# Kernel optimization log

Hardware: AMD Instinct MI355X
Metric: run time of the kernel (lower is better)

Reference implementation:

```python
import jax, jax.numpy as jnp
import numpy as np

NUM_HEADS = 8
NUM_LAYERS = 4
BASE_THR = 0.5     # AdaptiveLIF base_threshold (state reset -> no adaptation on single step)
TAU_MEM = 5.0      # tau_mem (single step from zero state: mem = decay*0 + x = x)
SURR_SLOPE = 5.0   # fast-sigmoid surrogate slope (forward path unaffected)
EPS = 1e-5
NEG = -1e9


@jax.custom_vjp
def spike(u):
    return (u > 0.0).astype(u.dtype)

def _spike_fwd(u):
    return (u > 0.0).astype(u.dtype), u

def _spike_bwd(u, g):
    return (g / (1.0 + SURR_SLOPE * jnp.abs(u)) ** 2,)

spike.defvjp(_spike_fwd, _spike_bwd)


def lif(x):
    # AdaptiveLIF, single timestep from reset state: mem = x, thr = base_threshold
    return spike(x - BASE_THR)


def layer_norm(x, g, b):
    m = jnp.mean(x, axis=-1, keepdims=True)
    v = jnp.mean((x - m) ** 2, axis=-1, keepdims=True)
    return (x - m) * jax.lax.rsqrt(v + EPS) * g + b


def dsa(x, wq, bq, wk, bk, wv, bv, wo, bo, top_k):
    # Dynamic Sparse Attention: dense scores -> per-query top-k mask -> softmax -> AV
    B, T, D = x.shape
    H = NUM_HEADS
    dh = D // H

    def heads(w, bias):
        return (x @ w.T + bias).reshape(B, T, H, dh).transpose(0, 2, 1, 3)  # [B,H,T,dh]

    q, k, v = heads(wq, bq), heads(wk, bk), heads(wv, bv)
    scores = jnp.einsum('bhqd,bhkd->bhqk', q, k) / jnp.sqrt(jnp.asarray(dh, x.dtype))
    vals, idx = jax.lax.top_k(scores, top_k)  # [B,H,T,K]

    # scatter top-k values into a -inf-filled score matrix (exact top-k sparsity)
    N = B * H * T
    rows = jnp.arange(N)[:, None]
    sp = jnp.full((N, T), NEG, scores.dtype).at[rows, idx.reshape(N, top_k)].set(vals.reshape(N, top_k))
    attn = jax.nn.softmax(sp.reshape(B, H, T, T), axis=-1)

    out = jnp.einsum('bhqk,bhkd->bhqd', attn, v)
    out = out.transpose(0, 2, 1, 3).reshape(B, T, D)
    out = out @ wo.T + bo
    return lif(out)  # spiking output of attention


def ffn(x, w1, b1, w2, b2):
    h = lif(x @ w1.T + b1)
    return lif(h @ w2.T + b2)


def setup_inputs() -> dict:
    key = jax.random.key(0)
    ks = jax.random.split(key, 16)
    L, D, F, IN, OUT, B, T = NUM_LAYERS, 512, 2048, 128, 256, 2, 2048
    s = 0.02
    return {
        'x': jax.random.normal(ks[0], (B, T, IN), jnp.float32),
        'emb_w': jax.random.normal(ks[1], (D, IN), jnp.float32) * s,
        'emb_b': jnp.zeros((D,), jnp.float32),
        'pos_emb': jax.random.normal(ks[2], (1, T, D), jnp.float32) * s,
        'wq': jax.random.normal(ks[3], (L, D, D), jnp.float32) * s,
        'bq': jnp.zeros((L, D), jnp.float32),
        'wk': jax.random.normal(ks[4], (L, D, D), jnp.float32) * s,
        'bk': jnp.zeros((L, D), jnp.float32),
        'wv': jax.random.normal(ks[5], (L, D, D), jnp.float32) * s,
        'bv': jnp.zeros((L, D), jnp.float32),
        'wo': jax.random.normal(ks[6], (L, D, D), jnp.float32) * s,
        'bo': jnp.zeros((L, D), jnp.float32),
        'ln1_g': jnp.ones((L, D), jnp.float32),
        'ln1_b': jnp.zeros((L, D), jnp.float32),
        'fc1_w': jax.random.normal(ks[7], (L, F, D), jnp.float32) * s,
        'fc1_b': jnp.zeros((L, F), jnp.float32),
        'fc2_w': jax.random.normal(ks[8], (L, D, F), jnp.float32) * s,
        'fc2_b': jnp.zeros((L, D), jnp.float32),
        'ln2_g': jnp.ones((L, D), jnp.float32),
        'ln2_b': jnp.zeros((L, D), jnp.float32),
        'fnorm_g': jnp.ones((D,), jnp.float32),
        'fnorm_b': jnp.zeros((D,), jnp.float32),
        'cls_w': jax.random.normal(ks[9], (OUT, D), jnp.float32) * s,
        'cls_b': jnp.zeros((OUT,), jnp.float32),
        'top_k': 32,
    }


def reference(x, emb_w, emb_b, pos_emb, wq, bq, wk, bk, wv, bv, wo, bo,
              ln1_g, ln1_b, fc1_w, fc1_b, fc2_w, fc2_b, ln2_g, ln2_b,
              fnorm_g, fnorm_b, cls_w, cls_b, top_k):
    B, T, _ = x.shape
    h = x @ emb_w.T + emb_b + pos_emb[:, :T, :]
    for l in range(NUM_LAYERS):
        a = dsa(h, wq[l], bq[l], wk[l], bk[l], wv[l], bv[l], wo[l], bo[l], top_k)
        h = layer_norm(h + a, ln1_g[l], ln1_b[l])
        f = ffn(h, fc1_w[l], fc1_b[l], fc2_w[l], fc2_b[l])
        h = layer_norm(h + f, ln2_g[l], ln2_b[l])
    h = layer_norm(h, fnorm_g, fnorm_b)
    pooled = jnp.mean(h, axis=1)  # [B, D]
    return pooled @ cls_w.T + cls_b
```

## Files before the change

### kernel.cpp

```cpp
#include <hip/hip_runtime.h>
#include <math.h>
#include <float.h>

#define T_SEQ  2048
#define DMODEL 512
#define NHEAD  8
#define DHEAD  64
#define FDIM   2048
#define NLAYER 4
#define NB     2
#define MROWS  (NB*T_SEQ)

typedef _Float16 f16x8 __attribute__((ext_vector_type(8)));
typedef float    f32x4 __attribute__((ext_vector_type(4)));

__device__ __forceinline__ void async16(const _Float16* g, _Float16* l) {
    __builtin_amdgcn_global_load_lds(
        (const __attribute__((address_space(1))) unsigned int*)g,
        (__attribute__((address_space(3))) unsigned int*)l, 16, 0, 0);
}

template<int BN, int EPI>
__global__ __launch_bounds__(256) void gemm_k(
    const float* __restrict__ A, const float* __restrict__ W,
    const float* __restrict__ bias, const float* __restrict__ pos,
    float* __restrict__ C, int M, int N, int K)
{
    constexpr int BM = 128;
    constexpr int BK = 32;
    constexpr int MN = BN / 16;
    __shared__ float As[BK][BM + 4];
    __shared__ float Ws[BK][BN + 4];
    const int tid = threadIdx.x;
    const int n0 = blockIdx.x * BN;
    const int m0 = blockIdx.y * BM;
    const int tx = tid & 15;
    const int ty = tid >> 4;

    float acc[8][MN];
    #pragma unroll
    for (int i = 0; i < 8; ++i)
        #pragma unroll
        for (int j = 0; j < MN; ++j) acc[i][j] = 0.f;

    for (int k0 = 0; k0 < K; k0 += BK) {
        #pragma unroll
        for (int it = 0; it < 4; ++it) {
            int qq = tid + 256 * it;
            int m = qq >> 3, kq = qq & 7;
            float4 v4 = *(const float4*)(A + (size_t)(m0 + m) * K + k0 + kq * 4);
            As[kq*4+0][m] = v4.x; As[kq*4+1][m] = v4.y;
            As[kq*4+2][m] = v4.z; As[kq*4+3][m] = v4.w;
        }
        #pragma unroll
        for (int it = 0; it < BN/32; ++it) {
            int qq = tid + 256 * it;
            int n = qq >> 3, kq = qq & 7;
            float4 v4 = *(const float4*)(W + (size_t)(n0 + n) * K + k0 + kq * 4);
            Ws[kq*4+0][n] = v4.x; Ws[kq*4+1][n] = v4.y;
            Ws[kq*4+2][n] = v4.z; Ws[kq*4+3][n] = v4.w;
        }
        __syncthreads();
        for (int kk = 0; kk < BK; ++kk) {
            float a[8], b[MN];
            float4 a0 = *(const float4*)&As[kk][ty*8];
            float4 a1 = *(const float4*)&As[kk][ty*8+4];
            a[0]=a0.x; a[1]=a0.y; a[2]=a0.z; a[3]=a0.w;
            a[4]=a1.x; a[5]=a1.y; a[6]=a1.z; a[7]=a1.w;
            float4 b0 = *(const float4*)&Ws[kk][tx*4];
            b[0]=b0.x; b[1]=b0.y; b[2]=b0.z; b[3]=b0.w;
            if constexpr (MN == 8) {
                float4 b1 = *(const float4*)&Ws[kk][64 + tx*4];
                b[4]=b1.x; b[5]=b1.y; b[6]=b1.z; b[7]=b1.w;
            }
            #pragma unroll
            for (int i = 0; i < 8; ++i)
                #pragma unroll
                for (int j = 0; j < MN; ++j)
                    acc[i][j] = fmaf(a[i], b[j], acc[i][j]);
        }
        __syncthreads();
    }

    #pragma unroll
    for (int i = 0; i < 8; ++i) {
        int m = m0 + ty*8 + i;
        #pragma unroll
        for (int jb = 0; jb < MN/4; ++jb) {
            int nn = n0 + jb*64 + tx*4;
            float4 r;
            r.x = acc[i][jb*4+0] + bias[nn+0];
            r.y = acc[i][jb*4+1] + bias[nn+1];
            r.z = acc[i][jb*4+2] + bias[nn+2];
            r.w = acc[i][jb*4+3] + bias[nn+3];
            if constexpr (EPI == 1) {
                const float* pp = pos + (size_t)(m & (T_SEQ-1)) * DMODEL + nn;
                r.x += pp[0]; r.y += pp[1]; r.z += pp[2]; r.w += pp[3];
            }
            *(float4*)(C + (size_t)m * N + nn) = r;
        }
    }
}

template<int BM, int BN, int ASRC, int EPI, int LAYOUT>
__global__ __launch_bounds__(256, (BM == 64) ? 3 : 2) void mgemm_k(
    const _Float16* __restrict__ AH, const _Float16* __restrict__ AL,
    const _Float16* __restrict__ WH, const _Float16* __restrict__ WL,
    const float* __restrict__ bias,
    float* __restrict__ O0, float* __restrict__ O1, float* __restrict__ O2,
    float* __restrict__ O3, float* __restrict__ O4,
    int M, int N, int K)
{
    constexpr int MI = BM / 32;
    constexpr int NJ = BN / 32;
    __shared__ _Float16 AsH[2][4][BM][8];
    __shared__ _Float16 AsL[(ASRC == 0) ? 2 : 1][(ASRC == 0) ? 4 : 1][(ASRC == 0) ? BM : 1][8];
    __shared__ _Float16 WsH[2][4][BN][8];
    __shared__ _Float16 WsL[2][4][BN][8];

    const int tid = threadIdx.x;
    const int npan = N / BN;
    const int bid  = blockIdx.x;
    const int n0 = (bid % npan) * BN;
    const int m0 = (bid / npan) * BM;
    const int wv = tid >> 6, lane = tid & 63;
    const int mw = (wv >> 1) * (BM/2), nw = (wv & 1) * (BN/2);
    const int fr = lane & 15;
    const int kb = lane >> 4;

    const int wsrow = tid >> 1;
    const int wskb  = (tid & 1) * 2;
    const int wkoff = (tid & 1) * 16;
    const int arow  = tid >> 2, akb = tid & 3;

    f16x8 pa0, pa1, pal0, pal1, pw0, pw1, pwl0, pwl1;

    auto gload = [&](int k0) {
        if constexpr (BM == 128) {
            const _Float16* ap = AH + (size_t)(m0 + wsrow) * K + k0 + wkoff;
            pa0 = *(const f16x8*)ap;
            pa1 = *(const f16x8*)(ap + 8);
            if constexpr (ASRC == 0) {
                const _Float16* alp = AL + (size_t)(m0 + wsrow) * K + k0 + wkoff;
                pal0 = *(const f16x8*)alp;
                pal1 = *(const f16x8*)(alp + 8);
            }
        } else {
            pa0 = *(const f16x8*)(AH + (size_t)(m0 + arow) * K + k0 + akb*8);
            if constexpr (ASRC == 0)
                pal0 = *(const f16x8*)(AL + (size_t)(m0 + arow) * K + k0 + akb*8);
        }
        if constexpr (BN == 128) {
            const _Float16* wp = WH + (size_t)(n0 + wsrow) * K + k0 + wkoff;
            pw0 = *(const f16x8*)wp;
            pw1 = *(const f16x8*)(wp + 8);
            const _Float16* wlp = WL + (size_t)(n0 + wsrow) * K + k0 + wkoff;
            pwl0 = *(const f16x8*)wlp;
            pwl1 = *(const f16x8*)(wlp + 8);
        } else {
            pw0  = *(const f16x8*)(WH + (size_t)(n0 + arow) * K + k0 + akb*8);
            pwl0 = *(const f16x8*)(WL + (size_t)(n0 + arow) * K + k0 + akb*8);
        }
    };
    auto swrite = [&](int buf) {
        if constexpr (BM == 128) {
            *(f16x8*)&AsH[buf][wskb  ][wsrow][0] = pa0;
            *(f16x8*)&AsH[buf][wskb+1][wsrow][0] = pa1;
            if constexpr (ASRC == 0) {
                *(f16x8*)&AsL[buf][wskb  ][wsrow][0] = pal0;
                *(f16x8*)&AsL[buf][wskb+1][wsrow][0] = pal1;
            }
        } else {
            *(f16x8*)&AsH[buf][akb][arow][0] = pa0;
            if constexpr (ASRC == 0)
                *(f16x8*)&AsL[buf][akb][arow][0] = pal0;
        }
        if constexpr (BN == 128) {
            *(f16x8*)&WsH[buf][wskb  ][wsrow][0] = pw0;
            *(f16x8*)&WsH[buf][wskb+1][wsrow][0] = pw1;
            *(f16x8*)&WsL[buf][wskb  ][wsrow][0] = pwl0;
            *(f16x8*)&WsL[buf][wskb+1][wsrow][0] = pwl1;
        } else {
            *(f16x8*)&WsH[buf][akb][arow][0] = pw0;
            *(f16x8*)&WsL[buf][akb][arow][0] = pwl0;
        }
    };

    f32x4 acc[MI][NJ];
    #pragma unroll
    for (int i = 0; i < MI; ++i)
        #pragma unroll
        for (int j = 0; j < NJ; ++j) acc[i][j] = (f32x4)(0.f);

    const int NT = K >> 5;
    int cur = 0;
    gload(0);
    swrite(0);
    __syncthreads();

    for (int t = 0; t < NT; ++t) {
        const bool more = (t + 1 < NT);
        if (more) gload((t + 1) << 5);

        f16x8 aH[MI], aL[MI], bH[NJ], bL[NJ];
        #pragma unroll
        for (int i = 0; i < MI; ++i) {
            aH[i] = *(const f16x8*)&AsH[cur][kb][mw + i*16 + fr][0];
            if constexpr (ASRC == 0) aL[i] = *(const f16x8*)&AsL[cur][kb][mw + i*16 + fr][0];
        }
        #pragma unroll
        for (int j = 0; j < NJ; ++j) {
            bH[j] = *(const f16x8*)&WsH[cur][kb][nw + j*16 + fr][0];
            bL[j] = *(const f16x8*)&WsL[cur][kb][nw + j*16 + fr][0];
        }
        #pragma unroll
        for (int i = 0; i < MI; ++i)
            #pragma unroll
            for (int j = 0; j < NJ; ++j) {
                acc[i][j] = __builtin_amdgcn_mfma_f32_16x16x32_f16(aH[i], bH[j], acc[i][j], 0, 0, 0);
                acc[i][j] = __builtin_amdgcn_mfma_f32_16x16x32_f16(aH[i], bL[j], acc[i][j], 0, 0, 0);
                if constexpr (ASRC == 0)
                    acc[i][j] = __builtin_amdgcn_mfma_f32_16x16x32_f16(aL[i], bH[j], acc[i][j], 0, 0, 0);
            }
        if (more) {
            swrite(cur ^ 1);
            __syncthreads();
            cur ^= 1;
        }
    }

    const int qq = lane >> 4;
    #pragma unroll
    for (int j = 0; j < NJ; ++j) {
        int n = n0 + nw + j*16 + fr;
        float bv = bias[n];
        #pragma unroll
        for (int i = 0; i < MI; ++i) {
            #pragma unroll
            for (int r = 0; r < 4; ++r) {
                int m = m0 + mw + i*16 + qq*4 + r;
                float val = acc[i][j][r] * (1.f/1024.f) + bv;
                if constexpr (EPI == 2) val = val > 0.5f ? 1.f : 0.f;
                if constexpr (EPI == 3) {
                    ((_Float16*)O0)[(size_t)m * N + n] = (val > 0.5f) ? (_Float16)16.f : (_Float16)0.f;
                } else if constexpr (LAYOUT == 0) {
                    O0[(size_t)m * N + n] = val;
                } else {
                    int b_ = m >> 11, t_ = m & (T_SEQ-1);
                    if (n < 512) {
                        size_t hl = (((size_t)(b_*NHEAD + (n>>6))*T_SEQ + t_) << 6) + (n & 63);
                        float s16 = 16.f * val;
                        _Float16 hh = (_Float16)s16;
                        ((_Float16*)O0)[hl] = hh;
                        ((_Float16*)O1)[hl] = (_Float16)(s16 - (float)hh);
                    } else if (n < 1024) {
                        int nn = n - 512;
                        size_t hl = (((size_t)(b_*NHEAD + (nn>>6))*T_SEQ + t_) << 6) + (nn & 63);
                        float s16 = 16.f * val;
                        _Float16 hh = (_Float16)s16;
                        ((_Float16*)O2)[hl] = hh;
                        ((_Float16*)O3)[hl] = (_Float16)(s16 - (float)hh);
                    } else {
                        int nn = n - 1024;
                        O4[(((size_t)(b_*NHEAD + (nn>>6))*T_SEQ + t_) << 6) + (nn & 63)] = val;
                    }
                }
            }
        }
    }
}

__global__ __launch_bounds__(256) void cvtw_k(
    const float* __restrict__ w, _Float16* __restrict__ H, _Float16* __restrict__ L,
    int n, float scale)
{
    int i = blockIdx.x * 256 + threadIdx.x;
    if (i < n) {
        float s = scale * w[i];
        _Float16 h = (_Float16)s;
        H[i] = h;
        L[i] = (_Float16)(s - (float)h);
    }
}

__global__ __launch_bounds__(256) void cvtlayer_k(
    const float* __restrict__ wq, const float* __restrict__ wk, const float* __restrict__ wv,
    const float* __restrict__ bq, const float* __restrict__ bk, const float* __restrict__ bv,
    const float* __restrict__ wo, const float* __restrict__ f1w, const float* __restrict__ f2w,
    _Float16* __restrict__ WcatH, _Float16* __restrict__ WcatL, float* __restrict__ bcat,
    _Float16* __restrict__ WoH, _Float16* __restrict__ WoL,
    _Float16* __restrict__ W1H, _Float16* __restrict__ W1L,
    _Float16* __restrict__ W2H, _Float16* __restrict__ W2L)
{
    int i = blockIdx.x * 256 + threadIdx.x;
    float w;
    _Float16 *H, *L;
    int off;
    if (i < 786432) {
        int src = i >> 18, o = i & 262143;
        w = (src == 0 ? wq : (src == 1 ? wk : wv))[o];
        H = WcatH; L = WcatL; off = i;
    } else if (i < 1048576) {
        off = i - 786432;  w = wo[off];  H = WoH; L = WoL;
    } else if (i < 2097152) {
        off = i - 1048576; w = f1w[off]; H = W1H; L = W1L;
    } else if (i < 3145728) {
        off = i - 2097152; w = f2w[off]; H = W2H; L = W2L;
    } else if (i < 3145728 + 1536) {
        int j = i - 3145728;
        int src = j >> 9, o = j & 511;
        bcat[j] = (src == 0 ? bq : (src == 1 ? bk : bv))[o];
        return;
    } else return;
    float s = 64.f * w;
    _Float16 h = (_Float16)s;
    H[off] = h;
    L[off] = (_Float16)(s - (float)h);
}

__global__ __launch_bounds__(512, 4) void attn_k(
    const _Float16* __restrict__ qH, const _Float16* __restrict__ qL,
    const _Float16* __restrict__ kH, const _Float16* __restrict__ kL,
    const float* __restrict__ v,
    _Float16* __restrict__ outH, _Float16* __restrict__ outL)
{
    __shared__ unsigned char lds[66560];
    _Float16* ksH = (_Float16*)(lds);
    _Float16* ksL = (_Float16*)(lds + 16384);
    float    (*ss)[132] = (float(*)[132])(lds + 32768);
    float*   wrow       = (float*)(lds + 32768);
    int*     irow       = (int*)(lds + 32768 + 8448);

    const int tid = threadIdx.x;
    const int bh  = blockIdx.y;
    const int t0  = blockIdx.x * 64;
    const _Float16* qHb = qH + ((size_t)bh * T_SEQ + t0) * DHEAD;
    const _Float16* qLb = qL + ((size_t)bh * T_SEQ + t0) * DHEAD;
    const _Float16* kHb = kH + (size_t)bh * T_SEQ * DHEAD;
    const _Float16* kLb = kL + (size_t)bh * T_SEQ * DHEAD;
    const float*    vb  = v  + (size_t)bh * T_SEQ * DHEAD;

    unsigned kreg[32];
    #pragma unroll
    for (int i = 0; i < 32; ++i) kreg[i] = 0u;

    const int wv = tid >> 6, lane = tid & 63;
    const int fr = lane & 15, q4 = lane >> 4;
    const int mh  = (wv >> 2) * 32;
    const int c0w = (wv & 3) * 32;
    const int srow = tid >> 3;
    const int ssub = tid & 7;

    f16x8 qaH[2][2], qaL[2][2];
    #pragma unroll
    for (int ks = 0; ks < 2; ++ks) {
        const int doff = ks*32 + q4*8;
        qaH[ks][0] = *(const f16x8*)(qHb + (mh + fr)*DHEAD + doff);
        qaH[ks][1] = *(const f16x8*)(qHb + (mh + 16 + fr)*DHEAD + doff);
        qaL[ks][0] = *(const f16x8*)(qLb + (mh + fr)*DHEAD + doff);
        qaL[ks][1] = *(const f16x8*)(qLb + (mh + 16 + fr)*DHEAD + doff);
    }

    auto stage = [&](int jt) {
        const int j0 = jt * 128;
        #pragma unroll
        for (int i = 0; i < 2; ++i) {
            const int r0 = wv*16 + i*8;
            const int cc = r0 + (lane >> 3);
            const int ch = (lane & 7) ^ (cc & 7);
            const size_t goff = (size_t)(j0 + cc) * DHEAD + ch*8;
            async16(kHb + goff, ksH + r0*64);
            async16(kLb + goff, ksL + r0*64);
        }
    };

    stage(0);
    __syncthreads();

    for (int jt = 0; jt < 16; ++jt) {
        const int j0 = jt * 128;

        f32x4 acc[2][2];
        acc[0][0] = (f32x4)(0.f); acc[0][1] = (f32x4)(0.f);
        acc[1][0] = (f32x4)(0.f); acc[1][1] = (f32x4)(0.f);
        #pragma unroll
        for (int ks = 0; ks < 2; ++ks) {
            const int chq  = ks*4 + q4;
            #pragma unroll
            for (int nj = 0; nj < 2; ++nj) {
                const int cc = c0w + nj*16 + fr;
                const int sl = cc*64 + (chq ^ (cc & 7))*8;
                f16x8 bHf = *(const f16x8*)&ksH[sl];
                f16x8 bLf = *(const f16x8*)&ksL[sl];
                acc[0][nj] = __builtin_amdgcn_mfma_f32_16x16x32_f16(qaH[ks][0], bHf, acc[0][nj], 0, 0, 0);
                acc[0][nj] = __builtin_amdgcn_mfma_f32_16x16x32_f16(qaH[ks][0], bLf, acc[0][nj], 0, 0, 0);
                acc[0][nj] = __builtin_amdgcn_mfma_f32_16x16x32_f16(qaL[ks][0], bHf, acc[0][nj], 0, 0, 0);
                acc[1][nj] = __builtin_amdgcn_mfma_f32_16x16x32_f16(qaH[ks][1], bHf, acc[1][nj], 0, 0, 0);
                acc[1][nj] = __builtin_amdgcn_mfma_f32_16x16x32_f16(qaH[ks][1], bLf, acc[1][nj], 0, 0, 0);
                acc[1][nj] = __builtin_amdgcn_mfma_f32_16x16x32_f16(qaL[ks][1], bHf, acc[1][nj], 0, 0, 0);
            }
        }
        #pragma unroll
        for (int mi = 0; mi < 2; ++mi)
            #pragma unroll
            for (int nj = 0; nj < 2; ++nj)
                #pragma unroll
                for (int r = 0; r < 4; ++r)
                    ss[mh + mi*16 + q4*4 + r][c0w + nj*16 + fr] = acc[mi][nj][r] * (1.f/2048.f);
        __syncthreads();

        if (jt < 15) stage(jt + 1);

        float4 c4[4];
        {
            const float* ssr = &ss[srow][0] + ssub*4;
            #pragma unroll
            for (int g = 0; g < 4; ++g) c4[g] = *(const float4*)(ssr + g*32);
        }
        unsigned cand[16];
        #pragma unroll
        for (int g = 0; g < 4; ++g) {
            float vg[4] = {c4[g].x, c4[g].y, c4[g].z, c4[g].w};
            #pragma unroll
            for (int r = 0; r < 4; ++r) {
                unsigned u = __float_as_uint(vg[r]);
                u ^= (unsigned)((int)u >> 31) | 0x80000000u;
                int col = ssub*4 + g*32 + r;
                cand[g*4+r] = (u & 0xFFFFF800u) | (unsigned)(2047 - (j0 + col));
            }
        }
        #pragma unroll
        for (int k2 = 2; k2 <= 16; k2 <<= 1) {
            #pragma unroll
            for (int j2 = k2 >> 1; j2 > 0; j2 >>= 1) {
                #pragma unroll
                for (int i2 = 0; i2 < 16; ++i2) {
                    int l2 = i2 ^ j2;
                    if (l2 > i2) {
                        unsigned a = cand[i2], b = cand[l2];
                        unsigned mn = a < b ? a : b;
                        unsigned mx = a < b ? b : a;
                        if ((i2 & k2) == 0) { cand[i2] = mx; cand[l2] = mn; }
                        else                { cand[i2] = mn; cand[l2] = mx; }
                    }
                }
            }
        }
        #pragma unroll
        for (int j2 = 0; j2 < 16; ++j2) {
            unsigned b = cand[15 - j2];
            if (kreg[16 + j2] < b) kreg[16 + j2] = b;
        }
        #pragma unroll
        for (int st = 16; st >= 1; st >>= 1) {
            #pragma unroll
            for (int i2 = 0; i2 < 32; ++i2) {
                if ((i2 & st) == 0) {
                    unsigned lo = kreg[i2], hi = kreg[i2 | st];
                    kreg[i2]      = lo < hi ? hi : lo;
                    kreg[i2 | st] = lo < hi ? lo : hi;
                }
            }
        }
        __syncthreads();
    }

    #pragma unroll
    for (int s = 1; s <= 4; s <<= 1) {
        #pragma unroll
        for (int i = 0; i < 16; ++i) {
            unsigned pa = (unsigned)__shfl_xor((int)kreg[31-i], s, 64);
            unsigned pb = (unsigned)__shfl_xor((int)kreg[i],    s, 64);
            if (pa > kreg[i])    kreg[i]    = pa;
            if (pb > kreg[31-i]) kreg[31-i] = pb;
        }
        #pragma unroll
        for (int st = 16; st >= 1; st >>= 1) {
            #pragma unroll
            for (int i2 = 0; i2 < 32; ++i2) {
                if ((i2 & st) == 0) {
                    unsigned lo = kreg[i2], hi = kreg[i2 | st];
                    kreg[i2]      = lo < hi ? hi : lo;
                    kreg[i2 | st] = lo < hi ? lo : hi;
                }
            }
        }
    }

    if (ssub == 0) {
        float w[32];
        #pragma unroll
        for (int i = 0; i < 32; ++i) {
            unsigned um = kreg[i] & 0xFFFFF800u;
            unsigned ub = (um & 0x80000000u) ? (um ^ 0x80000000u) : ~um;
            w[i] = __uint_as_float(ub);
        }
        float m = w[0];
        float s = 0.f;
        #pragma unroll
        for (int i = 0; i < 32; ++i) { w[i] = __expf(w[i] - m); s += w[i]; }
        float inv = 1.f / s;
        #pragma unroll
        for (int i = 0; i < 32; ++i) {
            wrow[srow*33 + i] = w[i] * inv;
            irow[srow*33 + i] = 2047 - (int)(kreg[i] & 0x7FFu);
        }
    }
    __syncthreads();

    const int wid = tid >> 6, lane2 = tid & 63;
    const int b = bh >> 3, h = bh & 7;
    for (int rr = wid; rr < 64; rr += 8) {
        float a0 = 0.f, a1 = 0.f, a2 = 0.f, a3 = 0.f;
        #pragma unroll
        for (int i = 0; i < 8; ++i) {
            a0 = fmaf(wrow[rr*33 + i],      vb[(size_t)irow[rr*33 + i]      * DHEAD + lane2], a0);
            a1 = fmaf(wrow[rr*33 + 8 + i],  vb[(size_t)irow[rr*33 + 8 + i]  * DHEAD + lane2], a1);
            a2 = fmaf(wrow[rr*33 + 16 + i], vb[(size_t)irow[rr*33 + 16 + i] * DHEAD + lane2], a2);
            a3 = fmaf(wrow[rr*33 + 24 + i], vb[(size_t)irow[rr*33 + 24 + i] * DHEAD + lane2], a3);
        }
        float accv = (a0 + a1) + (a2 + a3);
        size_t oi = ((size_t)(b * T_SEQ + t0 + rr)) * DMODEL + h * DHEAD + lane2;
        float s16 = 16.f * accv;
        _Float16 hh = (_Float16)s16;
        outH[oi] = hh;
        outL[oi] = (_Float16)(s16 - (float)hh);
    }
}

__global__ __launch_bounds__(256) void ln_k(
    const float* __restrict__ x, const float* __restrict__ res,
    const float* __restrict__ g, const float* __restrict__ bb,
    float* __restrict__ out, _Float16* __restrict__ oH, _Float16* __restrict__ oL)
{
    __shared__ float red[8];
    const int row = blockIdx.x;
    const int tid = threadIdx.x;
    const float* xr = x + (size_t)row * DMODEL;
    float v0 = xr[tid], v1 = xr[tid + 256];
    if (res) {
        const float* rr = res + (size_t)row * DMODEL;
        v0 += rr[tid]; v1 += rr[tid + 256];
    }
    float s = v0 + v1;
    #pragma unroll
    for (int o = 1; o < 64; o <<= 1) s += __shfl_xor(s, o);
    const int wid = tid >> 6, lane = tid & 63;
    if (lane == 0) red[wid] = s;
    __syncthreads();
    float mean = (red[0] + red[1] + red[2] + red[3]) * (1.f / DMODEL);
    float d0 = v0 - mean, d1 = v1 - mean;
    float qs = d0*d0 + d1*d1;
    #pragma unroll
    for (int o = 1; o < 64; o <<= 1) qs += __shfl_xor(qs, o);
    if (lane == 0) red[4 + wid] = qs;
    __syncthreads();
    float var = (red[4] + red[5] + red[6] + red[7]) * (1.f / DMODEL);
    float rs = rsqrtf(var + 1e-5f);
    float o0 = d0 * rs * g[tid]       + bb[tid];
    float o1 = d1 * rs * g[tid + 256] + bb[tid + 256];
    size_t base = (size_t)row * DMODEL;
    out[base + tid]       = o0;
    out[base + tid + 256] = o1;
    float s0 = 16.f * o0, s1 = 16.f * o1;
    _Float16 h0 = (_Float16)s0, h1 = (_Float16)s1;
    oH[base + tid]       = h0;
    oH[base + tid + 256] = h1;
    oL[base + tid]       = (_Float16)(s0 - (float)h0);
    oL[base + tid + 256] = (_Float16)(s1 - (float)h1);
}

__global__ __launch_bounds__(256) void pool_k(
    const float* __restrict__ h, float* __restrict__ part)
{
    const int chunk = blockIdx.x & 15;
    const int idx = (blockIdx.x >> 4) * 256 + threadIdx.x;
    const int b = idx >> 9, d = idx & 511;
    const float* p = h + ((size_t)b * T_SEQ + chunk * 128) * DMODEL + d;
    float s = 0.f;
    for (int t = 0; t < 128; ++t) s += p[(size_t)t * DMODEL];
    part[chunk * 1024 + idx] = s;
}

__global__ __launch_bounds__(256) void poolsum_k(
    const float* __restrict__ part, float* __restrict__ pooled)
{
    int idx = blockIdx.x * 256 + threadIdx.x;
    float s = 0.f;
    #pragma unroll
    for (int c = 0; c < 16; ++c) s += part[c * 1024 + idx];
    pooled[idx] = s * (1.f / T_SEQ);
}

__global__ __launch_bounds__(256) void cls_k(
    const float* __restrict__ pooled, const float* __restrict__ w,
    const float* __restrict__ bias, float* __restrict__ out)
{
    const int wid = threadIdx.x >> 6, lane = threadIdx.x & 63;
    const int oi = blockIdx.x * 4 + wid;
    const int b = oi >> 8, o = oi & 255;
    const float* pr = pooled + b * DMODEL;
    const float* wr = w + (size_t)o * DMODEL;
    float s = 0.f;
    for (int d = lane; d < DMODEL; d += 64) s = fmaf(pr[d], wr[d], s);
    #pragma unroll
    for (int off = 1; off < 64; off <<= 1) s += __shfl_xor(s, off);
    if (lane == 0) out[oi] = s + bias[o];
}

extern "C" void kernel_launch(void* const* d_in, const int* in_sizes, int n_in,
                              void* d_out, int out_size, void* d_ws, size_t ws_size,
                              hipStream_t stream)
{
    const float* x     = (const float*)d_in[0];
    const float* emb_w = (const float*)d_in[1];
    const float* emb_b = (const float*)d_in[2];
    const float* pos   = (const float*)d_in[3];
    const float* wq    = (const float*)d_in[4];
    const float* bq    = (const float*)d_in[5];
    const float* wk    = (const float*)d_in[6];
    const float* bk    = (const float*)d_in[7];
    const float* wv    = (const float*)d_in[8];
    const float* bv    = (const float*)d_in[9];
    const float* wo    = (const float*)d_in[10];
    const float* bo    = (const float*)d_in[11];
    const float* ln1g  = (const float*)d_in[12];
    const float* ln1b  = (const float*)d_in[13];
    const float* fc1w  = (const float*)d_in[14];
    const float* fc1b  = (const float*)d_in[15];
    const float* fc2w  = (const float*)d_in[16];
    const float* fc2b  = (const float*)d_in[17];
    const float* ln2g  = (const float*)d_in[18];
    const float* ln2b  = (const float*)d_in[19];
    const float* fng   = (const float*)d_in[20];
    const float* fnb   = (const float*)d_in[21];
    const float* clsw  = (const float*)d_in[22];
    const float* clsb  = (const float*)d_in[23];

    float* ws = (float*)d_ws;
    const size_t SZ  = (size_t)MROWS * DMODEL;
    const size_t HP  = SZ / 2;
    float*     h     = ws;
    float*     t1    = ws + 1*SZ;
    _Float16*  hH    = (_Float16*)(ws + 2*SZ);
    _Float16*  hL    = (_Float16*)(ws + 2*SZ + HP);
    _Float16*  aoH   = (_Float16*)(ws + 3*SZ);
    _Float16*  aoL   = (_Float16*)(ws + 3*SZ + HP);
    _Float16*  qbH   = (_Float16*)(ws + 4*SZ);
    _Float16*  qbL   = (_Float16*)(ws + 4*SZ + HP);
    _Float16*  kbH   = (_Float16*)(ws + 5*SZ);
    _Float16*  kbL   = (_Float16*)(ws + 5*SZ + HP);
    float*     vbuf  = ws + 6*SZ;
    _Float16*  WcatH = (_Float16*)(ws + 7*SZ);
    _Float16*  WcatL = (_Float16*)(ws + 7*SZ + 393216);
    _Float16*  WoH   = (_Float16*)(ws + 7*SZ + 786432);
    _Float16*  WoL   = (_Float16*)(ws + 7*SZ + 917504);
    _Float16*  W1H   = (_Float16*)(ws + 7*SZ + 1048576);
    _Float16*  W1L   = (_Float16*)(ws + 7*SZ + 1572864);
    _Float16*  W2H   = (_Float16*)(ws + 7*SZ + 2097152);
    _Float16*  W2L   = (_Float16*)(ws + 7*SZ + 2621440);
    float*     bcat  = ws + 7*SZ + 3145728;
    float*     pooled= ws + 7*SZ + 3145728 + 1536;
    float*     part  = ws + 7*SZ + 3145728 + 1536 + 1024;
    _Float16*  hid   = (_Float16*)(ws + 4*SZ);
    const size_t needed = (7*SZ + 3145728 + 1536 + 1024 + 16384) * sizeof(float);
    if (ws_size < needed) return;

    dim3 blk(256);

    gemm_k<64,1><<<dim3(DMODEL/64, MROWS/128), blk, 0, stream>>>(
        x, emb_w, emb_b, pos, h, MROWS, DMODEL, 128);
    cvtw_k<<<dim3((int)(SZ/256)), blk, 0, stream>>>(h, hH, hL, (int)SZ, 16.f);

    for (int l = 0; l < NLAYER; ++l) {
        const float* wq_l = wq + (size_t)l*DMODEL*DMODEL;
        const float* bq_l = bq + (size_t)l*DMODEL;
        const float* wk_l = wk + (size_t)l*DMODEL*DMODEL;
        const float* bk_l = bk + (size_t)l*DMODEL;
        const float* wv_l = wv + (size_t)l*DMODEL*DMODEL;
        const float* bv_l = bv + (size_t)l*DMODEL;
        const float* wo_l = wo + (size_t)l*DMODEL*DMODEL;
        const float* bo_l = bo + (size_t)l*DMODEL;
        const float* f1w_l = fc1w + (size_t)l*FDIM*DMODEL;
        const float* f1b_l = fc1b + (size_t)l*FDIM;
        const float* f2w_l = fc2w + (size_t)l*DMODEL*FDIM;
        const float* f2b_l = fc2b + (size_t)l*DMODEL;

        cvtlayer_k<<<dim3(12294), blk, 0, stream>>>(
            wq_l, wk_l, wv_l, bq_l, bk_l, bv_l, wo_l, f1w_l, f2w_l,
            WcatH, WcatL, bcat, WoH, WoL, W1H, W1L, W2H, W2L);

        mgemm_k<64,128,0,0,2><<<dim3(768), blk, 0, stream>>>(
            hH, hL, WcatH, WcatL, bcat,
            (float*)qbH, (float*)qbL, (float*)kbH, (float*)kbL, vbuf,
            MROWS, 1536, DMODEL);

        attn_k<<<dim3(T_SEQ/64, NB*NHEAD), dim3(512), 0, stream>>>(
            qbH, qbL, kbH, kbL, vbuf, aoH, aoL);

        mgemm_k<64,64,0,2,0><<<dim3(512), blk, 0, stream>>>(
            aoH, aoL, WoH, WoL, bo_l, t1, nullptr, nullptr, nullptr, nullptr,
            MROWS, DMODEL, DMODEL);
        ln_k<<<dim3(MROWS), blk, 0, stream>>>(h, t1, ln1g + (size_t)l*DMODEL,
                                              ln1b + (size_t)l*DMODEL, h, hH, hL);

        mgemm_k<128,128,0,3,0><<<dim3(512), blk, 0, stream>>>(
            hH, hL, W1H, W1L, f1b_l, (float*)hid, nullptr, nullptr, nullptr, nullptr,
            MROWS, FDIM, DMODEL);
        mgemm_k<64,64,1,2,0><<<dim3(512), blk, 0, stream>>>(
            hid, nullptr, W2H, W2L, f2b_l, t1, nullptr, nullptr, nullptr, nullptr,
            MROWS, DMODEL, FDIM);
        ln_k<<<dim3(MROWS), blk, 0, stream>>>(h, t1, ln2g + (size_t)l*DMODEL,
                                              ln2b + (size_t)l*DMODEL, h, hH, hL);
    }

    ln_k<<<dim3(MROWS), blk, 0, stream>>>(h, nullptr, fng, fnb, h, hH, hL);
    pool_k<<<dim3(64), blk, 0, stream>>>(h, part);
    poolsum_k<<<dim3(4), blk, 0, stream>>>(part, pooled);
    cls_k<<<dim3(128), blk, 0, stream>>>(pooled, clsw, clsb, (float*)d_out);
}
```

Before: 1.118 ms.

## Pre-tile weights in k-blocked layout and stage W tiles via async global-to-LDS loads

The weight conversion kernel now writes fp16 hi/lo weights in a [K/8][N][8] blocked layout, so each wave's slab of a W tile is contiguous in global memory. The GEMM then loads W tiles straight into LDS with global_load_lds async copies instead of going through registers and separate shared stores. This is meant to cut register pressure and the VGPR-to-LDS write traffic for the weight operand, and to let those loads overlap with MFMA work. The A operand keeps the old register-staged path. Correctness now depends on the async copies having finished before the existing barrier and on the new layout matching the indexing every weight consumer uses.

```diff
diff --git a/kernel.cpp b/kernel.cpp
--- a/kernel.cpp
+++ b/kernel.cpp
@@ -133,9 +133,20 @@
     const int wkoff = (tid & 1) * 16;
     const int arow  = tid >> 2, akb = tid & 3;
 
-    f16x8 pa0, pa1, pal0, pal1, pw0, pw1, pwl0, pwl1;
-
-    auto gload = [&](int k0) {
+    f16x8 pa0, pa1, pal0, pal1;
+
+    auto stageW = [&](int k0, int buf) {
+        const size_t base = ((size_t)((k0 >> 3) + wv) * N + n0) * 8;
+        const _Float16* sH = WH + base + (size_t)lane * 8;
+        const _Float16* sL = WL + base + (size_t)lane * 8;
+        async16(sH, &WsH[buf][wv][0][0]);
+        async16(sL, &WsL[buf][wv][0][0]);
+        if constexpr (BN == 128) {
+            async16(sH + 512, &WsH[buf][wv][64][0]);
+            async16(sL + 512, &WsL[buf][wv][64][0]);
+        }
+    };
+    auto gloadA = [&](int k0) {
         if constexpr (BM == 128) {
             const _Float16* ap = AH + (size_t)(m0 + wsrow) * K + k0 + wkoff;
             pa0 = *(const f16x8*)ap;
@@ -150,19 +161,8 @@
             if constexpr (ASRC == 0)
                 pal0 = *(const f16x8*)(AL + (size_t)(m0 + arow) * K + k0 + akb*8);
         }
-        if constexpr (BN == 128) {
-            const _Float16* wp = WH + (size_t)(n0 + wsrow) * K + k0 + wkoff;
-            pw0 = *(const f16x8*)wp;
-            pw1 = *(const f16x8*)(wp + 8);
-            const _Float16* wlp = WL + (size_t)(n0 + wsrow) * K + k0 + wkoff;
-            pwl0 = *(const f16x8*)wlp;
-            pwl1 = *(const f16x8*)(wlp + 8);
-        } else {
-            pw0  = *(const f16x8*)(WH + (size_t)(n0 + arow) * K + k0 + akb*8);
-            pwl0 = *(const f16x8*)(WL + (size_t)(n0 + arow) * K + k0 + akb*8);
-        }
     };
-    auto swrite = [&](int buf) {
+    auto swriteA = [&](int buf) {
         if constexpr (BM == 128) {
             *(f16x8*)&AsH[buf][wskb  ][wsrow][0] = pa0;
             *(f16x8*)&AsH[buf][wskb+1][wsrow][0] = pa1;
@@ -175,15 +175,6 @@
             if constexpr (ASRC == 0)
                 *(f16x8*)&AsL[buf][akb][arow][0] = pal0;
         }
-        if constexpr (BN == 128) {
-            *(f16x8*)&WsH[buf][wskb  ][wsrow][0] = pw0;
-            *(f16x8*)&WsH[buf][wskb+1][wsrow][0] = pw1;
-            *(f16x8*)&WsL[buf][wskb  ][wsrow][0] = pwl0;
-            *(f16x8*)&WsL[buf][wskb+1][wsrow][0] = pwl1;
-        } else {
-            *(f16x8*)&WsH[buf][akb][arow][0] = pw0;
-            *(f16x8*)&WsL[buf][akb][arow][0] = pwl0;
-        }
     };
 
     f32x4 acc[MI][NJ];
@@ -194,13 +185,17 @@
 
     const int NT = K >> 5;
     int cur = 0;
-    gload(0);
-    swrite(0);
+    stageW(0, 0);
+    gloadA(0);
+    swriteA(0);
     __syncthreads();
 
     for (int t = 0; t < NT; ++t) {
         const bool more = (t + 1 < NT);
-        if (more) gload((t + 1) << 5);
+        if (more) {
+            stageW((t + 1) << 5, cur ^ 1);
+            gloadA((t + 1) << 5);
+        }
 
         f16x8 aH[MI], aL[MI], bH[NJ], bL[NJ];
         #pragma unroll
@@ -223,7 +218,7 @@
                     acc[i][j] = __builtin_amdgcn_mfma_f32_16x16x32_f16(aL[i], bH[j], acc[i][j], 0, 0, 0);
             }
         if (more) {
-            swrite(cur ^ 1);
+            swriteA(cur ^ 1);
             __syncthreads();
             cur ^= 1;
         }
@@ -297,15 +292,35 @@
     _Float16 *H, *L;
     int off;
     if (i < 786432) {
-        int src = i >> 18, o = i & 262143;
-        w = (src == 0 ? wq : (src == 1 ? wk : wv))[o];
-        H = WcatH; L = WcatL; off = i;
+        int j = i;
+        int kbq = j / 12288;
+        int rem = j - kbq * 12288;
+        int n = rem >> 3;
+        int k = kbq * 8 + (j & 7);
+        int sm = n >> 9, nn = n & 511;
+        w = (sm == 0 ? wq : (sm == 1 ? wk : wv))[nn * 512 + k];
+        H = WcatH; L = WcatL; off = j;
     } else if (i < 1048576) {
-        off = i - 786432;  w = wo[off];  H = WoH; L = WoL;
+        int j = i - 786432;
+        int kbq = j >> 12;
+        int n = (j >> 3) & 511;
+        int k = (kbq << 3) | (j & 7);
+        w = wo[n * 512 + k];
+        H = WoH; L = WoL; off = j;
     } else if (i < 2097152) {
-        off = i - 1048576; w = f1w[off]; H = W1H; L = W1L;
+        int j = i - 1048576;
+        int kbq = j >> 14;
+        int n = (j >> 3) & 2047;
+        int k = (kbq << 3) | (j & 7);
+        w = f1w[n * 512 + k];
+        H = W1H; L = W1L; off = j;
     } else if (i < 3145728) {
-        off = i - 2097152; w = f2w[off]; H = W2H; L = W2L;
+        int j = i - 2097152;
+        int kbq = j >> 12;
+        int n = (j >> 3) & 511;
+        int k = (kbq << 3) | (j & 7);
+        w = f2w[n * 2048 + k];
+        H = W2H; L = W2L; off = j;
     } else if (i < 3145728 + 1536) {
         int j = i - 3145728;
         int src = j >> 9, o = j & 511;
```

Result: faster. 1.094 ms (-2.1%).
